# Performance work log

Measured on AMD Instinct MI355X. Metric: run time of the kernel, lower is better.

The kernel has to match this reference:

```python
import jax, jax.numpy as jnp
import numpy as np

FILTER_SIZE = 4      # pooled output size (wH = wW = 4)
STRIDE = 16          # feature stride -> spatial_scale = 1/16
C = 512              # feature_dim
H = W = 22           # feature map size (352px crop / stride 16)
NI, NS = 3, 64       # images_in_sequence, sequences
KCELLS = 6           # static bound on integer cells overlapped per bin per axis


def setup_inputs() -> dict:
    key = jax.random.key(0)
    k1, k2, k3, k4 = jax.random.split(key, 4)
    feat = jax.random.normal(k1, (NI, NS, C, H, W), dtype=jnp.float32)
    # bb = (x, y, w, h) in image coords; keep boxes inside 352px image
    xy = jax.random.uniform(k2, (NI, NS, 2), minval=0.0, maxval=96.0)
    wh = jax.random.uniform(k3, (NI, NS, 2), minval=64.0, maxval=224.0)
    bb = jnp.concatenate([xy, wh], axis=-1).astype(jnp.float32)
    # conv init: normal(0, sqrt(2/(k*k*out_ch))), zero bias (as in the torch module)
    std = np.float32(np.sqrt(2.0 / (3 * 3 * C)))
    conv_w = jax.random.normal(k4, (C, C, 3, 3), dtype=jnp.float32) * std
    conv_b = jnp.zeros((C,), jnp.float32)
    return {"feat": feat, "bb": bb, "conv_w": conv_w, "conv_b": conv_b}


def _axis_weights(start, end, size):
    """Exact PrRoIPool 1D integration weights on integer grid points.
    start, end: (N, P) continuous bin boundaries in feature coords.
    Returns (N, P, size) weights s.t. integral of the piecewise-linear
    interpolant over [start, end] = sum_i w[i] * f(i)."""
    N, P = start.shape
    s0 = jnp.floor(start).astype(jnp.int32)                  # first cell
    cell = s0[..., None] + jnp.arange(KCELLS, dtype=jnp.int32)  # (N,P,K)
    cf = cell.astype(start.dtype)
    a1 = jnp.maximum(start[..., None], cf)                   # cell-bin intersection
    a2 = jnp.maximum(jnp.minimum(end[..., None], cf + 1.0), a1)
    alpha = a1 - cf
    lim = a2 - cf
    # integral of (1-t) and t over [alpha, lim]  (PrRoIPoolingMatCalculation)
    f0 = (lim - 0.5 * lim * lim) - (alpha - 0.5 * alpha * alpha)  # weight at point `cell`
    f1 = 0.5 * lim * lim - 0.5 * alpha * alpha                    # weight at `cell+1`
    idx0, idx1 = cell, cell + 1
    v0 = (idx0 >= 0) & (idx0 < size)   # out-of-bounds feature reads are 0
    v1 = (idx1 >= 0) & (idx1 < size)
    wts = jnp.concatenate([jnp.where(v0, f0, 0.0), jnp.where(v1, f1, 0.0)], -1)
    idx = jnp.concatenate([jnp.clip(idx0, 0, size - 1), jnp.clip(idx1, 0, size - 1)], -1)
    out = jnp.zeros((N, P, size), start.dtype)
    n_i = jnp.arange(N)[:, None, None]
    p_i = jnp.arange(P)[None, :, None]
    return out.at[n_i, p_i, idx].add(wts)


def prroi_pool(feat, rois, pooled, scale):
    """Precise RoI pooling. feat: (N,C,H,W); rois: (N,4) = (x1,y1,x2,y2),
    image coords; roi i pools from image i. Returns (N,C,pooled,pooled)."""
    x1, y1, x2, y2 = (rois[:, k] * scale for k in range(4))
    bin_w = (x2 - x1) / pooled
    bin_h = (y2 - y1) / pooled
    p = jnp.arange(pooled, dtype=feat.dtype)
    sh = y1[:, None] + p * bin_h[:, None]; eh = sh + bin_h[:, None]   # (N,P)
    sw = x1[:, None] + p * bin_w[:, None]; ew = sw + bin_w[:, None]
    Wy = _axis_weights(sh, eh, feat.shape[2])   # (N,P,H)
    Wx = _axis_weights(sw, ew, feat.shape[3])   # (N,P,W)
    acc = jnp.einsum('nph,nqw,nchw->ncpq', Wy, Wx, feat)
    area = jnp.maximum(bin_h * bin_w, 0.0)[:, None, None, None]
    return jnp.where(area == 0, 0.0, acc / jnp.where(area == 0, 1.0, area))


def reference(feat, bb, conv_w, conv_b):
    ni = feat.shape[0]
    x = feat.reshape(-1, C, H, W)
    x = jax.lax.conv_general_dilated(
        x, conv_w, window_strides=(1, 1), padding=((1, 1), (1, 1)),
        dimension_numbers=('NCHW', 'OIHW', 'NCHW')) + conv_b[None, :, None, None]
    b = bb.reshape(-1, 4)
    rois = jnp.concatenate([b[:, :2], b[:, :2] + b[:, 2:]], axis=-1)  # xyxy
    w = prroi_pool(x, rois, FILTER_SIZE, 1.0 / STRIDE)
    w = w.reshape(ni, -1, C, FILTER_SIZE, FILTER_SIZE).mean(axis=0)   # mean over images
    return w / (C * FILTER_SIZE * FILTER_SIZE)                        # filter_norm
```

## Files before the change

### kernel.cpp

```cpp
#include <hip/hip_runtime.h>


#define NIMG 192
#define CCH 512
#define FH 22
#define FW 22
#define SPATIAL 484
#define KDIM 4608
#define NDIM 1024
#define KQ 8
#define KSEG 576
#define CISTRIDE 1968
#define POOLBLKS 2048

typedef __bf16 bf16;
typedef __bf16 bf16x2 __attribute__((ext_vector_type(2)));
typedef __bf16 bf16x8 __attribute__((ext_vector_type(8)));
typedef float f32x2 __attribute__((ext_vector_type(2)));
typedef float f32x4 __attribute__((ext_vector_type(4)));

#define GLOBAL_AS __attribute__((address_space(1)))
#define LDS_AS __attribute__((address_space(3)))

__device__ __forceinline__ void gload_lds16(const void* g, void* l) {
  __builtin_amdgcn_global_load_lds((GLOBAL_AS const void*)g, (LDS_AS void*)l, 16, 0, 0);
}

#define LBAR()                                                   \
  do {                                                           \
    asm volatile("s_waitcnt lgkmcnt(0)" ::: "memory");           \
    __builtin_amdgcn_s_barrier();                                \
  } while (0)
#define FBAR()                                                   \
  do {                                                           \
    asm volatile("s_waitcnt vmcnt(0) lgkmcnt(0)" ::: "memory");  \
    __builtin_amdgcn_s_barrier();                                \
  } while (0)

__device__ __forceinline__ void axis_range(float a0, float aw, int& r0, int& r1) {
  const float scale = 1.f / 16.f;
  float s1 = a0 * scale;
  float s2 = (a0 + aw) * scale;
  float bl = (s2 - s1) * 0.25f;
  float endv = (s1 + 3 * bl) + bl;
  int c0 = max(0, (int)floorf(s1));
  int c1 = min(21, (int)floorf(endv) + 1);
  r0 = max(0, c0 - 1);
  r1 = min(21, c1 + 1);
}

__device__ __forceinline__ float axis_sum(float a0, float aw, int bin) {
  const float scale = 1.f / 16.f;
  float s1 = a0 * scale;
  float s2 = (a0 + aw) * scale;
  float blen = (s2 - s1) * 0.25f;
  float start = s1 + bin * blen;
  float end = start + blen;
  float inv = 1.0f / blen;
  float S = 0.f;
  int s0i = (int)floorf(start);
  for (int kk = 0; kk < 6; ++kk) {
    int cell = s0i + kk;
    float cf = (float)cell;
    float a1 = fmaxf(start, cf);
    float a2 = fmaxf(fminf(end, cf + 1.f), a1);
    float alpha = a1 - cf, lim = a2 - cf;
    float f0 = (lim - 0.5f * lim * lim) - (alpha - 0.5f * alpha * alpha);
    float f1 = 0.5f * lim * lim - 0.5f * alpha * alpha;
    if (cell >= 0 && cell < 22) S += f0 * inv;
    if (cell + 1 >= 0 && cell + 1 < 22) S += f1 * inv;
  }
  return S;
}

__global__ __launch_bounds__(256, 4) void pool_feat_kernel(
    const float* __restrict__ feat, const float* __restrict__ bb,
    const float* __restrict__ cw, bf16* __restrict__ Wb,
    bf16* __restrict__ Gb) {
  __shared__ __align__(16) char tileb[16 * CISTRIDE];
  __shared__ float wyl3[3 * 264];
  __shared__ float wxl3[3 * 264];
  int t = threadIdx.x;
  if (blockIdx.x >= POOLBLKS) {
    int co = blockIdx.x - POOLBLKS;
    float* lw = (float*)tileb;
    const float* src = cw + (long)co * CCH * 9;
    #pragma unroll
    for (int k = 0; k < 18; ++k) lw[t + 256 * k] = src[t + 256 * k];
    __syncthreads();
    bf16* dst = Wb + (long)co * 9 * CCH;
    #pragma unroll
    for (int k = 0; k < 18; ++k) {
      int f = t + 256 * k;
      int pos = f >> 9;
      int ci = f & 511;
      dst[f] = (bf16)lw[ci * 9 + pos];
    }
    return;
  }
  int s = blockIdx.x >> 5;
  int ciq = blockIdx.x & 31;
  int p = t >> 6;
  int lane = t & 63;
  int ci16 = lane & 15;
  int vq = lane >> 4;

  int yr0a[3], yr1a[3], xr0a[3], xr1a[3];
  #pragma unroll
  for (int i = 0; i < 3; ++i) {
    int n = i * 64 + s;
    axis_range(bb[n * 4 + 1], bb[n * 4 + 3], yr0a[i], yr1a[i]);
    axis_range(bb[n * 4 + 0], bb[n * 4 + 2], xr0a[i], xr1a[i]);
  }

  f32x4 A[9];
  #pragma unroll
  for (int a = 0; a < 9; ++a) A[a] = (f32x4){0.f, 0.f, 0.f, 0.f};
  const float* tf = (const float*)tileb;

  auto STAGE = [&](int img) {
    int n = img * 64 + s;
    int start16 = (yr0a[img] * 88) & ~15;
    int end16 = ((yr1a[img] + 1) * 88 + 15) & ~15;
    int cpi = (end16 - start16 + 1023) >> 10;
    const float* fpl0 = feat + ((long)n * CCH + ciq * 16) * SPATIAL;
    for (int k = p; k < 16 * cpi; k += 4) {
      int ci = (cpi == 2) ? (k >> 1) : k;
      int c = (cpi == 2) ? (k & 1) : 0;
      int cs = (c == cpi - 1) ? end16 - 1024 : start16;
      if (cs < 0) cs = 0;
      gload_lds16((const char*)(fpl0 + (long)ci * SPATIAL) + cs + lane * 16,
                  tileb + ci * CISTRIDE + cs + lane * 16);
    }
  };

  auto COMPUTE = [&](int img) {
    int yr0 = yr0a[img], yr1 = yr1a[img];
    int vbase = xr0a[img] & ~1;
    int npairs = ((xr1a[img] - vbase) >> 1) + 1;
    const float* wy = wyl3 + img * 264;
    const f32x4* wx = (const f32x4*)(wxl3 + img * 264);
    const f32x2* pl2 = (const f32x2*)(tf + ci16 * (CISTRIDE / 4));
    for (int j = vq; j < npairs; j += 4) {
      int vg = vbase + 2 * j;
      float a00 = 0.f, a01 = 0.f, a10 = 0.f, a11 = 0.f, a20 = 0.f, a21 = 0.f;
      for (int u = yr0; u <= yr1; ++u) {
        f32x2 f = pl2[(u * FW + vg) >> 1];
        float w0 = wy[u * 4 + p];
        float w1 = wy[(22 + u) * 4 + p];
        float w2 = wy[(44 + u) * 4 + p];
        a00 = fmaf(w0, f[0], a00); a01 = fmaf(w0, f[1], a01);
        a10 = fmaf(w1, f[0], a10); a11 = fmaf(w1, f[1], a11);
        a20 = fmaf(w2, f[0], a20); a21 = fmaf(w2, f[1], a21);
      }
      #pragma unroll
      for (int kx = 0; kx < 3; ++kx) {
        f32x4 wx0 = wx[kx * 22 + vg];
        f32x4 wx1 = wx[kx * 22 + vg + 1];
        A[kx] += wx0 * a00 + wx1 * a01;
        A[3 + kx] += wx0 * a10 + wx1 * a11;
        A[6 + kx] += wx0 * a20 + wx1 * a21;
      }
    }
  };

  STAGE(0);
  for (int idx = t; idx < 1584; idx += 256)
    (idx < 792 ? wyl3[idx] : wxl3[idx - 792]) = 0.f;
  LBAR();
  if (t < 24) {
    int img = t >> 3;
    int axis = (t >> 2) & 1;
    int bin = t & 3;
    int n = img * 64 + s;
    const float scale = 1.f / 16.f;
    float a0 = axis ? bb[n * 4 + 0] : bb[n * 4 + 1];
    float aw = axis ? bb[n * 4 + 2] : bb[n * 4 + 3];
    float s1 = a0 * scale;
    float s2 = (a0 + aw) * scale;
    float blen = (s2 - s1) * 0.25f;
    float start = s1 + bin * blen;
    float end = start + blen;
    float inv = 1.0f / blen;
    float* tbl = (axis ? wxl3 : wyl3) + img * 264;
    int s0i = (int)floorf(start);
    for (int kk = 0; kk < 6; ++kk) {
      int cell = s0i + kk;
      float cf = (float)cell;
      float a1 = fmaxf(start, cf);
      float a2 = fmaxf(fminf(end, cf + 1.f), a1);
      float alpha = a1 - cf, lim = a2 - cf;
      float f0 = (lim - 0.5f * lim * lim) - (alpha - 0.5f * alpha * alpha);
      float f1 = 0.5f * lim * lim - 0.5f * alpha * alpha;
      if (cell >= 0 && cell < 22) {
        float w = f0 * inv;
        #pragma unroll
        for (int ky = 0; ky < 3; ++ky) {
          int u = cell + ky - 1;
          if (u >= 0 && u < 22) tbl[(ky * 22 + u) * 4 + bin] += w;
        }
      }
      if (cell + 1 >= 0 && cell + 1 < 22) {
        float w = f1 * inv;
        #pragma unroll
        for (int ky = 0; ky < 3; ++ky) {
          int u = cell + ky;
          if (u >= 0 && u < 22) tbl[(ky * 22 + u) * 4 + bin] += w;
        }
      }
    }
  }
  FBAR();
  COMPUTE(0);
  #pragma unroll 1
  for (int img = 1; img < 3; ++img) {
    LBAR();
    STAGE(img);
    FBAR();
    COMPUTE(img);
  }

  #pragma unroll
  for (int pos = 0; pos < 9; ++pos) {
    #pragma unroll
    for (int q = 0; q < 4; ++q) {
      A[pos][q] += __shfl_xor(A[pos][q], 16);
      A[pos][q] += __shfl_xor(A[pos][q], 32);
    }
  }
  if (vq == 0) {
    int ci = ciq * 16 + ci16;
    #pragma unroll
    for (int pos = 0; pos < 9; ++pos)
      #pragma unroll
      for (int q = 0; q < 4; ++q)
        Gb[(long)(s * 16 + p * 4 + q) * KDIM + pos * CCH + ci] = (bf16)A[pos][q];
  }
}

__global__ __launch_bounds__(256, 2) void gemm_kernel(const bf16* __restrict__ Wb,
                                                      const bf16* __restrict__ Gb,
                                                      float* __restrict__ Opart) {
  __shared__ __align__(16) bf16 As[128 * 64];
  __shared__ __align__(16) bf16 Bs[64 * 64];
  int bid = blockIdx.x;
  int kq = bid & 7;
  int nt = (bid >> 3) & 15;
  int mt = bid >> 7;
  int co0 = mt << 7;
  int n0 = nt << 6;
  int kbase = kq * KSEG;

  int tid = threadIdx.x;
  int wv = tid >> 6, l = tid & 63;
  int wm = wv >> 1, wn = wv & 1;
  int lrow = l >> 3;
  int cg8 = ((l & 7) ^ lrow) << 3;

  long aOff[4], bOff[2];
  #pragma unroll
  for (int j = 0; j < 4; ++j) {
    int row = j * 32 + wv * 8 + lrow;
    aOff[j] = (long)(co0 + row) * KDIM + kbase + cg8;
  }
  #pragma unroll
  for (int j = 0; j < 2; ++j) {
    int row = j * 32 + wv * 8 + lrow;
    bOff[j] = (long)(n0 + row) * KDIM + kbase + cg8;
  }

  const f32x4 vz = {0.f, 0.f, 0.f, 0.f};
  f32x4 acc[4][2];
  #pragma unroll
  for (int a = 0; a < 4; ++a)
    #pragma unroll
    for (int b = 0; b < 2; ++b) acc[a][b] = vz;

  for (int c = 0; c < 9; ++c) {
    long sh = c * 64;
    #pragma unroll
    for (int j = 0; j < 4; ++j)
      gload_lds16(Wb + aOff[j] + sh, (char*)As + (j * 32 + wv * 8) * 128);
    #pragma unroll
    for (int j = 0; j < 2; ++j)
      gload_lds16(Gb + bOff[j] + sh, (char*)Bs + (j * 32 + wv * 8) * 128);
    __syncthreads();
    bf16x8 af[2][4], bfv[2][2];
    #pragma unroll
    for (int kk = 0; kk < 2; ++kk) {
      #pragma unroll
      for (int i = 0; i < 4; ++i) {
        int rowa = wm * 64 + i * 16 + (l & 15);
        int offa = rowa * 128 + kk * 64 + ((l >> 4) * 16);
        offa ^= (rowa & 7) << 4;
        af[kk][i] = *(const bf16x8*)((const char*)As + offa);
      }
      #pragma unroll
      for (int i = 0; i < 2; ++i) {
        int rowb = wn * 32 + i * 16 + (l & 15);
        int offb = rowb * 128 + kk * 64 + ((l >> 4) * 16);
        offb ^= (rowb & 7) << 4;
        bfv[kk][i] = *(const bf16x8*)((const char*)Bs + offb);
      }
    }
    #pragma unroll
    for (int kk = 0; kk < 2; ++kk)
      #pragma unroll
      for (int mi = 0; mi < 4; ++mi)
        #pragma unroll
        for (int nj = 0; nj < 2; ++nj)
          acc[mi][nj] = __builtin_amdgcn_mfma_f32_16x16x32_bf16(
              af[kk][mi], bfv[kk][nj], acc[mi][nj], 0, 0, 0);
    __syncthreads();
  }

  float* op = Opart + (long)kq * CCH * NDIM;
  #pragma unroll
  for (int nj = 0; nj < 2; ++nj) {
    int nn = n0 + wn * 32 + nj * 16 + (l & 15);
    #pragma unroll
    for (int mi = 0; mi < 4; ++mi) {
      #pragma unroll
      for (int rr = 0; rr < 4; ++rr) {
        int co = co0 + wm * 64 + mi * 16 + (l >> 4) * 4 + rr;
        op[(long)co * NDIM + nn] = acc[mi][nj][rr];
      }
    }
  }
}

__global__ __launch_bounds__(256) void epi_kernel(const float* __restrict__ Opart,
                                                  const float* __restrict__ bb,
                                                  const float* __restrict__ cb,
                                                  float* __restrict__ out) {
  __shared__ float bfl[16];
  int bid = blockIdx.x;
  int t = threadIdx.x;
  int s = bid >> 3;
  if (t < 16) {
    int p = t >> 2;
    int q = t & 3;
    float acc = 0.f;
    #pragma unroll
    for (int i = 0; i < 3; ++i) {
      int n = i * 64 + s;
      acc += axis_sum(bb[n * 4 + 1], bb[n * 4 + 3], p) *
             axis_sum(bb[n * 4 + 0], bb[n * 4 + 2], q);
    }
    bfl[t] = acc;
  }
  __syncthreads();
  int base = (bid * 256 + t) * 4;
  int co = (base >> 4) & 511;
  int p = (base >> 2) & 3;
  long osrc = (long)co * NDIM + s * 16 + p * 4;
  f32x4 v = *(const f32x4*)(Opart + osrc);
  #pragma unroll
  for (int kq = 1; kq < KQ; ++kq)
    v += *(const f32x4*)(Opart + (long)kq * CCH * NDIM + osrc);
  f32x4 bf4 = {bfl[p * 4 + 0], bfl[p * 4 + 1], bfl[p * 4 + 2], bfl[p * 4 + 3]};
  const float fin = 1.f / (3.f * 512.f * 16.f);
  v = (v + cb[co] * bf4) * fin;
  *(f32x4*)(out + base) = v;
}

extern "C" void kernel_launch(void* const* d_in, const int* in_sizes, int n_in,
                              void* d_out, int out_size, void* d_ws, size_t ws_size,
                              hipStream_t stream) {
  const float* feat = (const float*)d_in[0];
  const float* bb = (const float*)d_in[1];
  const float* cw = (const float*)d_in[2];
  const float* cb = (const float*)d_in[3];
  float* out = (float*)d_out;

  const size_t WB_BYTES = (size_t)CCH * 9 * CCH * 2;
  const size_t GB_BYTES = (size_t)NDIM * KDIM * 2;
  const size_t OP_BYTES = (size_t)KQ * CCH * NDIM * 4;
  if (ws_size < WB_BYTES + GB_BYTES + OP_BYTES) return;

  char* ws = (char*)d_ws;
  bf16* Wb = (bf16*)ws;
  bf16* Gb = (bf16*)(ws + WB_BYTES);
  float* Opart = (float*)(ws + WB_BYTES + GB_BYTES);

  hipLaunchKernelGGL(pool_feat_kernel, dim3(POOLBLKS + CCH), dim3(256), 0, stream,
                     feat, bb, cw, Wb, Gb);
  hipLaunchKernelGGL(gemm_kernel, dim3(512), dim3(256), 0, stream, Wb, Gb, Opart);
  hipLaunchKernelGGL(epi_kernel, dim3(512), dim3(256), 0, stream, Opart, bb, cb, out);
}
```

Measured before the change: 69.78 us.

## Split pool compute across x-pairs with two bins per wave; store GEMM partials as bf16

The pooling kernel now has each wave handle two pooled rows and half of the x-pairs instead of one row and all pairs. Each feature load from LDS therefore feeds two bins' FMAs, and the two x-halves are combined through an LDS scratch reduction before writing Gb. Separately, the split-K GEMM partials are stored as bf16 rather than fp32, halving Opart write and read traffic in the GEMM and epilogue. The tradeoffs are extra registers (two accumulator sets), an added LDS reduction step, and reduced precision in the partial sums.

```diff
diff --git a/kernel.cpp b/kernel.cpp
--- a/kernel.cpp
+++ b/kernel.cpp
@@ -15,6 +15,7 @@
 
 typedef __bf16 bf16;
 typedef __bf16 bf16x2 __attribute__((ext_vector_type(2)));
+typedef __bf16 bf16x4 __attribute__((ext_vector_type(4)));
 typedef __bf16 bf16x8 __attribute__((ext_vector_type(8)));
 typedef float f32x2 __attribute__((ext_vector_type(2)));
 typedef float f32x4 __attribute__((ext_vector_type(4)));
@@ -100,10 +101,13 @@
   }
   int s = blockIdx.x >> 5;
   int ciq = blockIdx.x & 31;
-  int p = t >> 6;
+  int w = t >> 6;
+  int ph = w >> 1;
+  int vh = w & 1;
   int lane = t & 63;
   int ci16 = lane & 15;
-  int vq = lane >> 4;
+  int vsub = lane >> 4;
+  int vg8 = vh * 4 + vsub;
 
   int yr0a[3], yr1a[3], xr0a[3], xr1a[3];
   #pragma unroll
@@ -113,9 +117,12 @@
     axis_range(bb[n * 4 + 0], bb[n * 4 + 2], xr0a[i], xr1a[i]);
   }
 
-  f32x4 A[9];
-  #pragma unroll
-  for (int a = 0; a < 9; ++a) A[a] = (f32x4){0.f, 0.f, 0.f, 0.f};
+  f32x4 A0[9], A1[9];
+  #pragma unroll
+  for (int a = 0; a < 9; ++a) {
+    A0[a] = (f32x4){0.f, 0.f, 0.f, 0.f};
+    A1[a] = (f32x4){0.f, 0.f, 0.f, 0.f};
+  }
   const float* tf = (const float*)tileb;
 
   auto STAGE = [&](int img) {
@@ -124,7 +131,7 @@
     int end16 = ((yr1a[img] + 1) * 88 + 15) & ~15;
     int cpi = (end16 - start16 + 1023) >> 10;
     const float* fpl0 = feat + ((long)n * CCH + ciq * 16) * SPATIAL;
-    for (int k = p; k < 16 * cpi; k += 4) {
+    for (int k = w; k < 16 * cpi; k += 4) {
       int ci = (cpi == 2) ? (k >> 1) : k;
       int c = (cpi == 2) ? (k & 1) : 0;
       int cs = (c == cpi - 1) ? end16 - 1024 : start16;
@@ -141,25 +148,32 @@
     const float* wy = wyl3 + img * 264;
     const f32x4* wx = (const f32x4*)(wxl3 + img * 264);
     const f32x2* pl2 = (const f32x2*)(tf + ci16 * (CISTRIDE / 4));
-    for (int j = vq; j < npairs; j += 4) {
+    for (int j = vg8; j < npairs; j += 8) {
       int vg = vbase + 2 * j;
       float a00 = 0.f, a01 = 0.f, a10 = 0.f, a11 = 0.f, a20 = 0.f, a21 = 0.f;
+      float b00 = 0.f, b01 = 0.f, b10 = 0.f, b11 = 0.f, b20 = 0.f, b21 = 0.f;
       for (int u = yr0; u <= yr1; ++u) {
         f32x2 f = pl2[(u * FW + vg) >> 1];
-        float w0 = wy[u * 4 + p];
-        float w1 = wy[(22 + u) * 4 + p];
-        float w2 = wy[(44 + u) * 4 + p];
-        a00 = fmaf(w0, f[0], a00); a01 = fmaf(w0, f[1], a01);
-        a10 = fmaf(w1, f[0], a10); a11 = fmaf(w1, f[1], a11);
-        a20 = fmaf(w2, f[0], a20); a21 = fmaf(w2, f[1], a21);
+        f32x2 wk0 = *(const f32x2*)(wy + u * 4 + 2 * ph);
+        f32x2 wk1 = *(const f32x2*)(wy + (22 + u) * 4 + 2 * ph);
+        f32x2 wk2 = *(const f32x2*)(wy + (44 + u) * 4 + 2 * ph);
+        a00 = fmaf(wk0[0], f[0], a00); a01 = fmaf(wk0[0], f[1], a01);
+        a10 = fmaf(wk1[0], f[0], a10); a11 = fmaf(wk1[0], f[1], a11);
+        a20 = fmaf(wk2[0], f[0], a20); a21 = fmaf(wk2[0], f[1], a21);
+        b00 = fmaf(wk0[1], f[0], b00); b01 = fmaf(wk0[1], f[1], b01);
+        b10 = fmaf(wk1[1], f[0], b10); b11 = fmaf(wk1[1], f[1], b11);
+        b20 = fmaf(wk2[1], f[0], b20); b21 = fmaf(wk2[1], f[1], b21);
       }
       #pragma unroll
       for (int kx = 0; kx < 3; ++kx) {
         f32x4 wx0 = wx[kx * 22 + vg];
         f32x4 wx1 = wx[kx * 22 + vg + 1];
-        A[kx] += wx0 * a00 + wx1 * a01;
-        A[3 + kx] += wx0 * a10 + wx1 * a11;
-        A[6 + kx] += wx0 * a20 + wx1 * a21;
+        A0[kx] += wx0 * a00 + wx1 * a01;
+        A0[3 + kx] += wx0 * a10 + wx1 * a11;
+        A0[6 + kx] += wx0 * a20 + wx1 * a21;
+        A1[kx] += wx0 * b00 + wx1 * b01;
+        A1[3 + kx] += wx0 * b10 + wx1 * b11;
+        A1[6 + kx] += wx0 * b20 + wx1 * b21;
       }
     }
   };
@@ -193,19 +207,19 @@
       float f0 = (lim - 0.5f * lim * lim) - (alpha - 0.5f * alpha * alpha);
       float f1 = 0.5f * lim * lim - 0.5f * alpha * alpha;
       if (cell >= 0 && cell < 22) {
-        float w = f0 * inv;
+        float wv_ = f0 * inv;
         #pragma unroll
         for (int ky = 0; ky < 3; ++ky) {
           int u = cell + ky - 1;
-          if (u >= 0 && u < 22) tbl[(ky * 22 + u) * 4 + bin] += w;
+          if (u >= 0 && u < 22) tbl[(ky * 22 + u) * 4 + bin] += wv_;
         }
       }
       if (cell + 1 >= 0 && cell + 1 < 22) {
-        float w = f1 * inv;
+        float wv_ = f1 * inv;
         #pragma unroll
         for (int ky = 0; ky < 3; ++ky) {
           int u = cell + ky;
-          if (u >= 0 && u < 22) tbl[(ky * 22 + u) * 4 + bin] += w;
+          if (u >= 0 && u < 22) tbl[(ky * 22 + u) * 4 + bin] += wv_;
         }
       }
     }
@@ -224,23 +238,44 @@
   for (int pos = 0; pos < 9; ++pos) {
     #pragma unroll
     for (int q = 0; q < 4; ++q) {
-      A[pos][q] += __shfl_xor(A[pos][q], 16);
-      A[pos][q] += __shfl_xor(A[pos][q], 32);
-    }
-  }
-  if (vq == 0) {
+      A0[pos][q] += __shfl_xor(A0[pos][q], 16);
+      A0[pos][q] += __shfl_xor(A0[pos][q], 32);
+      A1[pos][q] += __shfl_xor(A1[pos][q], 16);
+      A1[pos][q] += __shfl_xor(A1[pos][q], 32);
+    }
+  }
+  __syncthreads();
+  f32x4* scr = (f32x4*)tileb;
+  if (vh == 1 && vsub == 0) {
+    int base = (ph * 16 + ci16) * 18;
+    #pragma unroll
+    for (int pos = 0; pos < 9; ++pos) {
+      scr[base + pos] = A0[pos];
+      scr[base + 9 + pos] = A1[pos];
+    }
+  }
+  __syncthreads();
+  if (vh == 0) {
+    int base = (ph * 16 + ci16) * 18;
     int ci = ciq * 16 + ci16;
-    #pragma unroll
-    for (int pos = 0; pos < 9; ++pos)
-      #pragma unroll
-      for (int q = 0; q < 4; ++q)
-        Gb[(long)(s * 16 + p * 4 + q) * KDIM + pos * CCH + ci] = (bf16)A[pos][q];
+    int p0 = ph * 2;
+    #pragma unroll
+    for (int pos = 0; pos < 9; ++pos) {
+      if ((pos & 3) != vsub) continue;
+      f32x4 v0 = A0[pos] + scr[base + pos];
+      f32x4 v1 = A1[pos] + scr[base + 9 + pos];
+      #pragma unroll
+      for (int q = 0; q < 4; ++q) {
+        Gb[(long)(s * 16 + p0 * 4 + q) * KDIM + pos * CCH + ci] = (bf16)v0[q];
+        Gb[(long)(s * 16 + (p0 + 1) * 4 + q) * KDIM + pos * CCH + ci] = (bf16)v1[q];
+      }
+    }
   }
 }
 
 __global__ __launch_bounds__(256, 2) void gemm_kernel(const bf16* __restrict__ Wb,
                                                       const bf16* __restrict__ Gb,
-                                                      float* __restrict__ Opart) {
+                                                      bf16* __restrict__ Opart) {
   __shared__ __align__(16) bf16 As[128 * 64];
   __shared__ __align__(16) bf16 Bs[64 * 64];
   int bid = blockIdx.x;
@@ -314,7 +349,7 @@
     __syncthreads();
   }
 
-  float* op = Opart + (long)kq * CCH * NDIM;
+  bf16* op = Opart + (long)kq * CCH * NDIM;
   #pragma unroll
   for (int nj = 0; nj < 2; ++nj) {
     int nn = n0 + wn * 32 + nj * 16 + (l & 15);
@@ -323,13 +358,13 @@
       #pragma unroll
       for (int rr = 0; rr < 4; ++rr) {
         int co = co0 + wm * 64 + mi * 16 + (l >> 4) * 4 + rr;
-        op[(long)co * NDIM + nn] = acc[mi][nj][rr];
-      }
-    }
-  }
-}
-
-__global__ __launch_bounds__(256) void epi_kernel(const float* __restrict__ Opart,
+        op[(long)co * NDIM + nn] = (bf16)acc[mi][nj][rr];
+      }
+    }
+  }
+}
+
+__global__ __launch_bounds__(256) void epi_kernel(const bf16* __restrict__ Opart,
                                                   const float* __restrict__ bb,
                                                   const float* __restrict__ cb,
                                                   float* __restrict__ out) {
@@ -354,10 +389,13 @@
   int co = (base >> 4) & 511;
   int p = (base >> 2) & 3;
   long osrc = (long)co * NDIM + s * 16 + p * 4;
-  f32x4 v = *(const f32x4*)(Opart + osrc);
-  #pragma unroll
-  for (int kq = 1; kq < KQ; ++kq)
-    v += *(const f32x4*)(Opart + (long)kq * CCH * NDIM + osrc);
+  f32x4 v = {0.f, 0.f, 0.f, 0.f};
+  #pragma unroll
+  for (int kq = 0; kq < KQ; ++kq) {
+    bf16x4 o = *(const bf16x4*)(Opart + (long)kq * CCH * NDIM + osrc);
+    #pragma unroll
+    for (int j = 0; j < 4; ++j) v[j] += (float)o[j];
+  }
   f32x4 bf4 = {bfl[p * 4 + 0], bfl[p * 4 + 1], bfl[p * 4 + 2], bfl[p * 4 + 3]};
   const float fin = 1.f / (3.f * 512.f * 16.f);
   v = (v + cb[co] * bf4) * fin;
@@ -375,13 +413,13 @@
 
   const size_t WB_BYTES = (size_t)CCH * 9 * CCH * 2;
   const size_t GB_BYTES = (size_t)NDIM * KDIM * 2;
-  const size_t OP_BYTES = (size_t)KQ * CCH * NDIM * 4;
+  const size_t OP_BYTES = (size_t)KQ * CCH * NDIM * 2;
   if (ws_size < WB_BYTES + GB_BYTES + OP_BYTES) return;
 
   char* ws = (char*)d_ws;
   bf16* Wb = (bf16*)ws;
   bf16* Gb = (bf16*)(ws + WB_BYTES);
-  float* Opart = (float*)(ws + WB_BYTES + GB_BYTES);
+  bf16* Opart = (bf16*)(ws + WB_BYTES + GB_BYTES);
 
   hipLaunchKernelGGL(pool_feat_kernel, dim3(POOLBLKS + CCH), dim3(256), 0, stream,
                      feat, bb, cw, Wb, Gb);
```

Result: slower. 72.60 us (+4.1%).
